# Optimization experiments

Measured on AMD Instinct MI355X. Metric: run time of the kernel, lower is better.

The kernel has to match this reference:

```python
import jax, jax.numpy as jnp
import numpy as np

B, TQ, TKV, D_MODEL, H, DQ, DV = 4, 2048, 2048, 1024, 16, 64, 64
DK = DQ

def setup_inputs() -> dict:
    key = jax.random.key(0)
    ks = jax.random.split(key, 8)
    s = 0.02
    return {
        "query_sequence": jax.random.normal(ks[0], (B, TQ, D_MODEL), jnp.float32),
        "key_value_sequence": jax.random.normal(ks[1], (B, TKV, D_MODEL), jnp.float32),
        "key_value_padding_mask": jnp.zeros((B, TKV), dtype=bool),
        "Wq": jax.random.normal(ks[2], (D_MODEL, H * DQ), jnp.float32) * s,
        "bq": jnp.zeros((H * DQ,), jnp.float32),
        "Wkv": jax.random.normal(ks[3], (D_MODEL, H * (DK + DV)), jnp.float32) * s,
        "bkv": jnp.zeros((H * (DK + DV),), jnp.float32),
        "Wo": jax.random.normal(ks[4], (H * DV, D_MODEL), jnp.float32) * s,
        "bo": jnp.zeros((D_MODEL,), jnp.float32),
        "apply_causal_mask": 1,
    }

def reference(query_sequence, key_value_sequence, key_value_padding_mask,
              Wq, bq, Wkv, bkv, Wo, bo, apply_causal_mask):
    b, tq, _ = query_sequence.shape
    tkv = key_value_sequence.shape[1]
    q = (query_sequence @ Wq + bq).reshape(b, tq, H, DQ)          # (B,Tq,H,Dq)
    kv = key_value_sequence @ Wkv + bkv
    k = kv[..., : H * DK].reshape(b, tkv, H, DK)                   # (B,Tkv,H,Dk)
    v = kv[..., H * DK :].reshape(b, tkv, H, DV)                   # (B,Tkv,H,Dv)
    scores = jnp.einsum("bqhd,bkhd->bhqk", q, k) / jnp.sqrt(jnp.float32(DK))
    neg_inf = jnp.float32(-jnp.inf)
    scores = jnp.where(key_value_padding_mask[:, None, None, :], neg_inf, scores)
    if apply_causal_mask:
        causal = jnp.tril(jnp.ones((tq, tkv), dtype=bool))
        scores = jnp.where(causal[None, None, :, :], scores, neg_inf)
    attn = jax.nn.softmax(scores, axis=-1)
    out = jnp.einsum("bhqk,bkhd->bqhd", attn, v).reshape(b, tq, H * DV)
    return out @ Wo + bo
```

## Files before the change

kernel.cpp:

```cpp
#include <hip/hip_runtime.h>
#include <hip/hip_bf16.h>

#define B_   4
#define TQ_  2048
#define TKV_ 2048
#define DM_  1024
#define H_   16
#define DH_  64

#define SC_FOLD 0.18033688011112042f

using f32x4  = __attribute__((ext_vector_type(4))) float;
using f32x16 = __attribute__((ext_vector_type(16))) float;
using s16x8  = __attribute__((ext_vector_type(8))) short;

static __device__ __forceinline__ unsigned short f2bf(float f) {
  union { float f; unsigned int u; } v; v.f = f;
  unsigned int r = v.u + 0x7FFFu + ((v.u >> 16) & 1u);
  return (unsigned short)(r >> 16);
}
static __device__ __forceinline__ unsigned int pk2(float a, float b) {
  unsigned int r;
  asm("v_cvt_pk_bf16_f32 %0, %1, %2" : "=v"(r) : "v"(a), "v"(b));
  return r;
}
static __device__ __forceinline__ float max3f(float a, float b, float c) {
  float r;
  asm("v_max3_f32 %0, %1, %2, %3" : "=v"(r) : "v"(a), "v"(b), "v"(c));
  return r;
}

#define GL16(g, l)                                                          \
  __builtin_amdgcn_global_load_lds(                                         \
      (const __attribute__((address_space(1))) unsigned int*)(g),           \
      (__attribute__((address_space(3))) unsigned int*)(l), 16, 0, 0)

__global__ __launch_bounds__(256) void k_transpose_cast(
    const float* __restrict__ W, unsigned short* __restrict__ WT, int K, int N,
    float scale) {
  __shared__ float t[64][65];
  int n0 = blockIdx.x * 64, k0 = blockIdx.y * 64;
  int tx = threadIdx.x & 63, ty = threadIdx.x >> 6;
#pragma unroll
  for (int i = 0; i < 64; i += 4)
    t[ty + i][tx] = W[(size_t)(k0 + ty + i) * N + n0 + tx];
  __syncthreads();
#pragma unroll
  for (int i = 0; i < 64; i += 4)
    WT[(size_t)(n0 + ty + i) * K + k0 + tx] = f2bf(t[tx][ty + i] * scale);
}

__global__ __launch_bounds__(256) void k_cast_bf16(
    const float* __restrict__ in, unsigned short* __restrict__ out, int n4) {
  for (int i = blockIdx.x * 256 + threadIdx.x; i < n4; i += gridDim.x * 256) {
    f32x4 v = *(const f32x4*)(in + (size_t)i * 4);
    unsigned long long u = (unsigned long long)pk2(v[0], v[1]) |
                           ((unsigned long long)pk2(v[2], v[3]) << 32);
    *(unsigned long long*)(out + (size_t)i * 4) = u;
  }
}

template <int MODE, int BN>
__global__ __launch_bounds__(512, 2) void k_gemm8(
    const unsigned short* __restrict__ A, const unsigned short* __restrict__ BT,
    const float* __restrict__ bias, float bscale, unsigned short* __restrict__ out_a,
    unsigned short* __restrict__ out_b, float* __restrict__ out_f, int Kd) {
  constexpr int NI = BN / 64;
  constexpr int NH = NI / 2;
  __shared__ __align__(16) unsigned short As[2 * 256 * 64];
  __shared__ __align__(16) unsigned short Bs[2 * BN * 64];
  const int tid = threadIdx.x, lane = tid & 63, w = tid >> 6;
  const int wm = w >> 2, wn = w & 3;

  int nwg = gridDim.x * gridDim.y;
  int bid = blockIdx.y * gridDim.x + blockIdx.x;
  int cpx = nwg >> 3;
  int sw = (bid & 7) * cpx + (bid >> 3);
  int bx = sw % gridDim.x, by = sw / gridDim.x;
  int m0 = by * 256, n0 = bx * BN;

  const int strow = tid >> 3;
  const int sx = ((tid & 7) << 4) ^ ((strow & 7) << 4);
  const char* gA = (const char*)(A + (size_t)(m0 + strow) * Kd) + sx;
  const char* gB = (const char*)(BT + (size_t)(n0 + strow) * Kd) + sx;
  char* lA = (char*)As;
  char* lB = (char*)Bs;

#define ST_A(bf, c, k0) \
  GL16(gA + ((size_t)(c) * 64 * Kd + (size_t)(k0)) * 2, lA + (bf) * 32768 + (c) * 8192 + tid * 16)
#define ST_B(bf, c, k0) \
  GL16(gB + ((size_t)(c) * 64 * Kd + (size_t)(k0)) * 2, lB + (bf) * (BN * 128) + (c) * 8192 + tid * 16)

  f32x4 acc[8][NI];
#pragma unroll
  for (int i = 0; i < 8; ++i)
#pragma unroll
    for (int j = 0; j < NI; ++j) acc[i][j] = (f32x4){0.f, 0.f, 0.f, 0.f};

  s16x8 afr[4][2], bfr[NI][2];
  const int arow = wm * 128 + (lane & 15);
  const int brow = wn * (NI * 16) + (lane & 15);
  const int fcol = (lane >> 4) * 16;

#define RD_A(bf, r) (*(const s16x8*)(lA + (bf) * 32768 + (r) * 128 + ((fcol + _kk * 64) ^ (((r) & 7) << 4))))
#define RD_B(bf, r) (*(const s16x8*)(lB + (bf) * (BN * 128) + (r) * 128 + ((fcol + _kk * 64) ^ (((r) & 7) << 4))))

  const int nT = Kd >> 6;

  ST_B(0, 0, 0); ST_B(0, 1, 0);
  if (BN == 256) { ST_B(0, 2, 0); ST_B(0, 3, 0); }
  ST_A(0, 0, 0); ST_A(0, 2, 0);
  ST_A(0, 1, 0); ST_A(0, 3, 0);
  asm volatile("s_waitcnt vmcnt(2)" ::: "memory");
  __builtin_amdgcn_s_barrier();

#pragma unroll 1
  for (int t = 0; t < nT; ++t) {
    const int cur = t & 1, nxt = cur ^ 1;
    const int k1 = (t + 1) << 6;
    const bool st = (t + 1 < nT);

#pragma unroll
    for (int mi = 0; mi < 4; ++mi)
#pragma unroll
      for (int _kk = 0; _kk < 2; ++_kk) afr[mi][_kk] = RD_A(cur, arow + mi * 16);
#pragma unroll
    for (int ni = 0; ni < NH; ++ni)
#pragma unroll
      for (int _kk = 0; _kk < 2; ++_kk) bfr[ni][_kk] = RD_B(cur, brow + ni * 16);
    if (st) { ST_B(nxt, 0, k1); ST_B(nxt, 1, k1); }
    __builtin_amdgcn_s_barrier();
    __builtin_amdgcn_s_setprio(1);
#pragma unroll
    for (int mi = 0; mi < 4; ++mi)
#pragma unroll
      for (int ni = 0; ni < NH; ++ni)
#pragma unroll
        for (int kk = 0; kk < 2; ++kk)
          acc[mi][ni] = __builtin_amdgcn_mfma_f32_16x16x32_bf16(afr[mi][kk], bfr[ni][kk], acc[mi][ni], 0, 0, 0);
    __builtin_amdgcn_s_setprio(0);
    __builtin_amdgcn_s_barrier();

#pragma unroll
    for (int ni = NH; ni < NI; ++ni)
#pragma unroll
      for (int _kk = 0; _kk < 2; ++_kk) bfr[ni][_kk] = RD_B(cur, brow + ni * 16);
    if (st) {
      if (BN == 256) { ST_B(nxt, 2, k1); ST_B(nxt, 3, k1); }
      else           { ST_A(nxt, 0, k1); ST_A(nxt, 2, k1); }
    }
    if (st) asm volatile("s_waitcnt vmcnt(4)" ::: "memory");
    else    asm volatile("s_waitcnt vmcnt(0)" ::: "memory");
    __builtin_amdgcn_s_barrier();
    __builtin_amdgcn_s_setprio(1);
#pragma unroll
    for (int mi = 0; mi < 4; ++mi)
#pragma unroll
      for (int ni = NH; ni < NI; ++ni)
#pragma unroll
        for (int kk = 0; kk < 2; ++kk)
          acc[mi][ni] = __builtin_amdgcn_mfma_f32_16x16x32_bf16(afr[mi][kk], bfr[ni][kk], acc[mi][ni], 0, 0, 0);
    __builtin_amdgcn_s_setprio(0);
    __builtin_amdgcn_s_barrier();

#pragma unroll
    for (int mi = 0; mi < 4; ++mi)
#pragma unroll
      for (int _kk = 0; _kk < 2; ++_kk) afr[mi][_kk] = RD_A(cur, arow + (mi + 4) * 16);
    if (st) {
      if (BN == 256) { ST_A(nxt, 0, k1); ST_A(nxt, 2, k1); }
      else           { ST_A(nxt, 1, k1); ST_A(nxt, 3, k1); }
    }
    __builtin_amdgcn_s_barrier();
    __builtin_amdgcn_s_setprio(1);
#pragma unroll
    for (int mi = 0; mi < 4; ++mi)
#pragma unroll
      for (int ni = 0; ni < NH; ++ni)
#pragma unroll
        for (int kk = 0; kk < 2; ++kk)
          acc[mi + 4][ni] = __builtin_amdgcn_mfma_f32_16x16x32_bf16(afr[mi][kk], bfr[ni][kk], acc[mi + 4][ni], 0, 0, 0);
    __builtin_amdgcn_s_setprio(0);
    __builtin_amdgcn_s_barrier();

    if (st && BN == 256) { ST_A(nxt, 1, k1); ST_A(nxt, 3, k1); }
    asm volatile("s_waitcnt vmcnt(2)" ::: "memory");
    __builtin_amdgcn_s_barrier();
    __builtin_amdgcn_s_setprio(1);
#pragma unroll
    for (int mi = 0; mi < 4; ++mi)
#pragma unroll
      for (int ni = NH; ni < NI; ++ni)
#pragma unroll
        for (int kk = 0; kk < 2; ++kk)
          acc[mi + 4][ni] = __builtin_amdgcn_mfma_f32_16x16x32_bf16(afr[mi][kk], bfr[ni][kk], acc[mi + 4][ni], 0, 0, 0);
    __builtin_amdgcn_s_setprio(0);
    __builtin_amdgcn_s_barrier();
  }

#pragma unroll
  for (int mi = 0; mi < 8; ++mi) {
#pragma unroll
    for (int ni = 0; ni < NI; ++ni) {
      int col = n0 + wn * (NI * 16) + ni * 16 + (lane & 15);
      int rbase = m0 + wm * 128 + mi * 16 + (lane >> 4) * 4;
      float bv = bias[col] * bscale;
      if (MODE == 1 && col >= H_ * DH_) {
        int c2 = col - H_ * DH_;
        int h = c2 >> 6, d = c2 & 63;
        int b = rbase >> 11, tt = rbase & 2047;
        union { unsigned short h4[4]; unsigned long long u; } p;
#pragma unroll
        for (int r = 0; r < 4; ++r) p.h4[r] = f2bf(acc[mi][ni][r] + bv);
        *(unsigned long long*)(out_b + ((((size_t)b * H_ + h) * DH_ + d) * TKV_ + tt)) = p.u;
      } else {
#pragma unroll
        for (int r = 0; r < 4; ++r) {
          float v = acc[mi][ni][r] + bv;
          int m = rbase + r;
          if (MODE == 0) {
            int b = m >> 11, tt = m & 2047;
            int h = col >> 6, d = col & 63;
            out_a[(((size_t)b * H_ + h) * TQ_ + tt) * DH_ + d] = f2bf(v);
          } else if (MODE == 1) {
            int b = m >> 11, tt = m & 2047;
            int h = col >> 6, d = col & 63;
            out_a[(((size_t)b * H_ + h) * TKV_ + tt) * DH_ + d] = f2bf(v);
          } else {
            out_f[(size_t)m * DM_ + col] = v;
          }
        }
      }
    }
  }
#undef ST_A
#undef ST_B
#undef RD_A
#undef RD_B
}

__global__ __launch_bounds__(256, 2) void k_attn(
    const unsigned short* __restrict__ Qb, const unsigned short* __restrict__ Kb,
    const unsigned short* __restrict__ Vtb, const unsigned char* __restrict__ mask,
    const int* __restrict__ cflag, unsigned short* __restrict__ Ob) {
  __shared__ __align__(16) unsigned short Kt[128 * 64];
  __shared__ __align__(16) unsigned short Vt[64 * 128];
  __shared__ float bias_lds[128];
  __shared__ float red[4][32];
  __shared__ int s_any;

  int bid = blockIdx.y * gridDim.x + blockIdx.x;
  int r8 = bid & 7, q8 = bid >> 3;
  int bh = r8 * 8 + (q8 >> 3);
  int bx = q8 & 7;

  int b = bh >> 4, h = bh & 15;
  int tid = threadIdx.x, lane = tid & 63, w = tid >> 6;
  int hi = lane >> 5, l31 = lane & 31, l7 = lane & 7;
  const unsigned short* Qp = Qb + (size_t)bh * TQ_ * DH_;
  const char* Kp = (const char*)(Kb + (size_t)bh * TKV_ * DH_);
  const char* Vp = (const char*)(Vtb + (size_t)bh * DH_ * TKV_);
  const unsigned char* mp = mask + (size_t)b * TKV_;
  int causal = cflag[0];
  char* kbase = (char*)Kt;
  char* vbase = (char*)Vt;

  int st_r4 = tid >> 2;
  int st_c4 = (tid & 3) * 16;
  s16x8 pKr[4], pVr[4];

#define LOAD_KV(kv0)                                                          \
  {                                                                           \
    _Pragma("unroll")                                                         \
    for (int p = 0; p < 4; ++p) {                                             \
      int krow = (p >> 1) * 64 + st_r4;                                       \
      int kx = st_c4 + (p & 1) * 64;                                          \
      pKr[p] = *(const s16x8*)(Kp + ((size_t)((kv0) + krow) * 128 + kx));     \
      int vx = st_c4 + p * 64;                                                \
      pVr[p] = *(const s16x8*)(Vp + (((size_t)st_r4 * TKV_ + (kv0)) * 2 + vx)); \
    }                                                                         \
  }
#define WRITE_KV()                                                            \
  {                                                                           \
    _Pragma("unroll")                                                         \
    for (int p = 0; p < 4; ++p) {                                             \
      int krow = (p >> 1) * 64 + st_r4;                                       \
      int kx = st_c4 + (p & 1) * 64;                                          \
      *(s16x8*)(kbase + krow * 128 + (kx ^ ((st_r4 & 7) << 4))) = pKr[p];     \
      int vx = st_c4 + p * 64;                                                \
      *(s16x8*)(vbase + st_r4 * 256 + (vx ^ ((st_r4 & 7) << 4))) = pVr[p];    \
    }                                                                         \
  }

  if (tid == 0) s_any = 0;
  __syncthreads();
  {
    int any = 0;
    for (int i = tid; i < TKV_; i += 256) any |= mp[i];
    if (any) s_any = 1;
  }
  __syncthreads();
  const int has_mask = s_any;

#pragma unroll 1
  for (int pass = 0; pass < 2; ++pass) {
    int qb = (pass ? (15 - bx) : bx) * 128;
    int qw = qb + w * 32;
    int qrow = qw + l31;

    s16x8 bQ[4];
#pragma unroll
    for (int kk = 0; kk < 4; ++kk)
      bQ[kk] = *(const s16x8*)(Qp + (size_t)qrow * DH_ + kk * 16 + hi * 8);

    f32x16 accO[2];
#pragma unroll
    for (int i = 0; i < 16; ++i) { accO[0][i] = 0.f; accO[1][i] = 0.f; }
    float m_run = -INFINITY, l_run = 0.f;

    int nT = (causal ? (qb + 128) : TKV_) >> 7;

    LOAD_KV(0);
    WRITE_KV();
    if (has_mask && tid < 128) bias_lds[tid] = mp[tid] ? -1e30f : 0.0f;
    __syncthreads();

#pragma unroll 1
    for (int it = 0; it < nT; ++it) {
      int kv0 = it << 7;
      if (it + 1 < nT) LOAD_KV(kv0 + 128);

      int nact = 4;
      if (causal) {
        int rem = qw + 31 - kv0;
        nact = rem < 0 ? 0 : ((rem >> 5) + 1);
        if (nact > 4) nact = 4;
      }

      if (nact > 0) {
        f32x16 sT[4];
        __builtin_amdgcn_s_setprio(1);
#pragma unroll
        for (int s = 0; s < 4; ++s) {
          if (s < nact) {
#pragma unroll
            for (int i = 0; i < 16; ++i) sT[s][i] = 0.f;
#pragma unroll
            for (int kk = 0; kk < 4; ++kk) {
              s16x8 aK = *(const s16x8*)(kbase + (s * 32 + l31) * 128 +
                                         ((kk * 32 + hi * 16) ^ (l7 << 4)));
              sT[s] = __builtin_amdgcn_mfma_f32_32x32x16_bf16(aK, bQ[kk], sT[s], 0, 0, 0);
            }
          }
        }
        __builtin_amdgcn_s_setprio(0);

        float a0 = -INFINITY, a1 = -INFINITY, a2 = -INFINITY, a3 = -INFINITY;
#pragma unroll
        for (int s = 0; s < 4; ++s) {
          if (s < nact) {
            int diag_s = causal && (kv0 + s * 32 + 31 > qw);
            if (diag_s || has_mask) {
#pragma unroll
              for (int r = 0; r < 16; ++r) {
                int kvloc = s * 32 + (r & 3) + 8 * (r >> 2) + 4 * hi;
                float sv = sT[s][r];
                if (has_mask) sv += bias_lds[kvloc];
                if (diag_s && (kv0 + kvloc) > qrow) sv = -1e30f;
                sT[s][r] = sv;
              }
            }
#pragma unroll
            for (int r = 0; r < 16; r += 4) {
              a0 = fmaxf(a0, sT[s][r + 0]); a1 = fmaxf(a1, sT[s][r + 1]);
              a2 = fmaxf(a2, sT[s][r + 2]); a3 = fmaxf(a3, sT[s][r + 3]);
            }
          }
        }
        float mx = max3f(max3f(a0, a1, a2), a3, -3.0e30f);
        mx = fmaxf(mx, __shfl_xor(mx, 32));

        if (!__all(mx - m_run <= 8.0f)) {
          float mnew = fmaxf(m_run, mx);
          float sc_o = exp2f(m_run - mnew);
          m_run = mnew;
          l_run *= sc_o;
          red[w][l31] = sc_o;
#pragma unroll
          for (int r = 0; r < 16; ++r) {
            float f = red[w][(r & 3) + 8 * (r >> 2) + 4 * hi];
            accO[0][r] *= f;
            accO[1][r] *= f;
          }
        }

        float s0acc = 0.f, s1acc = 0.f, s2acc = 0.f, s3acc = 0.f;
#pragma unroll
        for (int s = 0; s < 4; ++s) {
          if (s < nact) {
#pragma unroll
            for (int r = 0; r < 16; r += 4) {
              float p0 = exp2f(sT[s][r + 0] - m_run);
              float p1 = exp2f(sT[s][r + 1] - m_run);
              float p2 = exp2f(sT[s][r + 2] - m_run);
              float p3 = exp2f(sT[s][r + 3] - m_run);
              sT[s][r + 0] = p0; sT[s][r + 1] = p1;
              sT[s][r + 2] = p2; sT[s][r + 3] = p3;
              s0acc += p0; s1acc += p1; s2acc += p2; s3acc += p3;
            }
          }
        }
        float ls = (s0acc + s1acc) + (s2acc + s3acc);
        ls += __shfl_xor(ls, 32);
        l_run += ls;

#pragma unroll
        for (int c = 0; c < 8; ++c) {
          if ((c >> 1) < nact) {
            int s = c >> 1, kk = c & 1;
            unsigned int x0 = pk2(sT[s][8 * kk + 0], sT[s][8 * kk + 1]);
            unsigned int y0 = pk2(sT[s][8 * kk + 2], sT[s][8 * kk + 3]);
            unsigned int x1 = pk2(sT[s][8 * kk + 4], sT[s][8 * kk + 5]);
            unsigned int y1 = pk2(sT[s][8 * kk + 6], sT[s][8 * kk + 7]);
            unsigned int sx0 = __shfl_xor(x0, 32), sy0 = __shfl_xor(y0, 32);
            unsigned int sx1 = __shfl_xor(x1, 32), sy1 = __shfl_xor(y1, 32);
            union { unsigned int u[4]; s16x8 v; } pf;
            pf.u[0] = hi ? sx1 : x0;
            pf.u[1] = hi ? sy1 : y0;
            pf.u[2] = hi ? x1 : sx0;
            pf.u[3] = hi ? y1 : sy0;
            __builtin_amdgcn_s_setprio(1);
#pragma unroll
            for (int dt = 0; dt < 2; ++dt) {
              s16x8 vf = *(const s16x8*)(vbase + (dt * 32 + l31) * 256 +
                                         ((c * 32 + hi * 16) ^ (l7 << 4)));
              accO[dt] = __builtin_amdgcn_mfma_f32_32x32x16_bf16(pf.v, vf, accO[dt], 0, 0, 0);
            }
            __builtin_amdgcn_s_setprio(0);
          }
        }
      }

      __syncthreads();
      if (it + 1 < nT) {
        WRITE_KV();
        if (has_mask && tid < 128) bias_lds[tid] = mp[kv0 + 128 + tid] ? -1e30f : 0.0f;
      }
      __syncthreads();
    }

    red[w][l31] = 1.0f / l_run;
#pragma unroll
    for (int r = 0; r < 16; ++r) {
      int R = (r & 3) + 8 * (r >> 2) + 4 * hi;
      float f = red[w][R];
      int qg = qw + R;
      size_t base = ((size_t)b * TQ_ + qg) * DM_ + h * DH_ + l31;
      Ob[base] = f2bf(accO[0][r] * f);
      Ob[base + 32] = f2bf(accO[1][r] * f);
    }
  }
#undef LOAD_KV
#undef WRITE_KV
}

extern "C" void kernel_launch(void* const* d_in, const int* in_sizes, int n_in,
                              void* d_out, int out_size, void* d_ws, size_t ws_size,
                              hipStream_t stream) {
  const float* xq  = (const float*)d_in[0];
  const float* xkv = (const float*)d_in[1];
  const unsigned char* mask = (const unsigned char*)d_in[2];
  const float* Wq  = (const float*)d_in[3];
  const float* bq  = (const float*)d_in[4];
  const float* Wkv = (const float*)d_in[5];
  const float* bkv = (const float*)d_in[6];
  const float* Wo  = (const float*)d_in[7];
  const float* bo  = (const float*)d_in[8];
  const int* cflag = (const int*)d_in[9];
  float* out = (float*)d_out;

  char* ws = (char*)d_ws;
  unsigned short* WqT  = (unsigned short*)(ws);
  unsigned short* WkvT = (unsigned short*)(ws + ((size_t)2 << 20));
  unsigned short* WoT  = (unsigned short*)(ws + ((size_t)6 << 20));
  unsigned short* Qb   = (unsigned short*)(ws + ((size_t)8 << 20));
  unsigned short* Kb   = (unsigned short*)(ws + ((size_t)24 << 20));
  unsigned short* Vb   = (unsigned short*)(ws + ((size_t)40 << 20));
  unsigned short* Xr   = (unsigned short*)(ws + ((size_t)56 << 20));
  unsigned short* Ob   = Xr;

  k_transpose_cast<<<dim3(16, 16), 256, 0, stream>>>(Wq, WqT, 1024, 1024, SC_FOLD);
  k_transpose_cast<<<dim3(32, 16), 256, 0, stream>>>(Wkv, WkvT, 1024, 2048, 1.0f);
  k_transpose_cast<<<dim3(16, 16), 256, 0, stream>>>(Wo, WoT, 1024, 1024, 1.0f);

  k_cast_bf16<<<2048, 256, 0, stream>>>(xq, Xr, B_ * TQ_ * DM_ / 4);
  k_gemm8<0, 128><<<dim3(8, 32), 512, 0, stream>>>(Xr, WqT, bq, SC_FOLD, Qb, nullptr, nullptr, 1024);

  k_cast_bf16<<<2048, 256, 0, stream>>>(xkv, Xr, B_ * TKV_ * DM_ / 4);
  k_gemm8<1, 256><<<dim3(8, 32), 512, 0, stream>>>(Xr, WkvT, bkv, 1.0f, Kb, Vb, nullptr, 1024);

  k_attn<<<dim3(8, B_ * H_), 256, 0, stream>>>(Qb, Kb, Vb, mask, cflag, Ob);

  k_gemm8<2, 128><<<dim3(8, 32), 512, 0, stream>>>(Ob, WoT, bo, 1.0f, nullptr, nullptr, out, 1024);
}
```

Baseline: 200.5 us.

## Read K/V fragments directly from global memory instead of staging through LDS

Removes the shared-memory staging of K and V tiles (register prefetch, swizzled LDS writes, and two block barriers per iteration) in the attention kernel. Each wave now loads its MFMA operand fragments straight from global memory and skips inactive causal tiles with a per-wave continue. This drops barrier and LDS traffic and frees LDS for occupancy, but each of the four waves re-fetches the same K/V data from global/L2, with no software prefetch to hide latency.

New measurement: 264.1 us. +31.7%, slower.

```diff
diff --git a/kernel.cpp b/kernel.cpp
--- a/kernel.cpp
+++ b/kernel.cpp
@@ -243,9 +243,6 @@
     const unsigned short* __restrict__ Qb, const unsigned short* __restrict__ Kb,
     const unsigned short* __restrict__ Vtb, const unsigned char* __restrict__ mask,
     const int* __restrict__ cflag, unsigned short* __restrict__ Ob) {
-  __shared__ __align__(16) unsigned short Kt[128 * 64];
-  __shared__ __align__(16) unsigned short Vt[64 * 128];
-  __shared__ float bias_lds[128];
   __shared__ float red[4][32];
   __shared__ int s_any;
 
@@ -256,41 +253,12 @@
 
   int b = bh >> 4, h = bh & 15;
   int tid = threadIdx.x, lane = tid & 63, w = tid >> 6;
-  int hi = lane >> 5, l31 = lane & 31, l7 = lane & 7;
+  int hi = lane >> 5, l31 = lane & 31;
   const unsigned short* Qp = Qb + (size_t)bh * TQ_ * DH_;
-  const char* Kp = (const char*)(Kb + (size_t)bh * TKV_ * DH_);
-  const char* Vp = (const char*)(Vtb + (size_t)bh * DH_ * TKV_);
+  const unsigned short* Kp = Kb + (size_t)bh * TKV_ * DH_;
+  const unsigned short* Vp = Vtb + (size_t)bh * DH_ * TKV_;
   const unsigned char* mp = mask + (size_t)b * TKV_;
   int causal = cflag[0];
-  char* kbase = (char*)Kt;
-  char* vbase = (char*)Vt;
-
-  int st_r4 = tid >> 2;
-  int st_c4 = (tid & 3) * 16;
-  s16x8 pKr[4], pVr[4];
-
-#define LOAD_KV(kv0)                                                          \
-  {                                                                           \
-    _Pragma("unroll")                                                         \
-    for (int p = 0; p < 4; ++p) {                                             \
-      int krow = (p >> 1) * 64 + st_r4;                                       \
-      int kx = st_c4 + (p & 1) * 64;                                          \
-      pKr[p] = *(const s16x8*)(Kp + ((size_t)((kv0) + krow) * 128 + kx));     \
-      int vx = st_c4 + p * 64;                                                \
-      pVr[p] = *(const s16x8*)(Vp + (((size_t)st_r4 * TKV_ + (kv0)) * 2 + vx)); \
-    }                                                                         \
-  }
-#define WRITE_KV()                                                            \
-  {                                                                           \
-    _Pragma("unroll")                                                         \
-    for (int p = 0; p < 4; ++p) {                                             \
-      int krow = (p >> 1) * 64 + st_r4;                                       \
-      int kx = st_c4 + (p & 1) * 64;                                          \
-      *(s16x8*)(kbase + krow * 128 + (kx ^ ((st_r4 & 7) << 4))) = pKr[p];     \
-      int vx = st_c4 + p * 64;                                                \
-      *(s16x8*)(vbase + st_r4 * 256 + (vx ^ ((st_r4 & 7) << 4))) = pVr[p];    \
-    }                                                                         \
-  }
 
   if (tid == 0) s_any = 0;
   __syncthreads();
@@ -320,15 +288,9 @@
 
     int nT = (causal ? (qb + 128) : TKV_) >> 7;
 
-    LOAD_KV(0);
-    WRITE_KV();
-    if (has_mask && tid < 128) bias_lds[tid] = mp[tid] ? -1e30f : 0.0f;
-    __syncthreads();
-
 #pragma unroll 1
     for (int it = 0; it < nT; ++it) {
       int kv0 = it << 7;
-      if (it + 1 < nT) LOAD_KV(kv0 + 128);
 
       int nact = 4;
       if (causal) {
@@ -336,117 +298,109 @@
         nact = rem < 0 ? 0 : ((rem >> 5) + 1);
         if (nact > 4) nact = 4;
       }
-
-      if (nact > 0) {
-        f32x16 sT[4];
-        __builtin_amdgcn_s_setprio(1);
-#pragma unroll
-        for (int s = 0; s < 4; ++s) {
-          if (s < nact) {
-#pragma unroll
-            for (int i = 0; i < 16; ++i) sT[s][i] = 0.f;
-#pragma unroll
-            for (int kk = 0; kk < 4; ++kk) {
-              s16x8 aK = *(const s16x8*)(kbase + (s * 32 + l31) * 128 +
-                                         ((kk * 32 + hi * 16) ^ (l7 << 4)));
-              sT[s] = __builtin_amdgcn_mfma_f32_32x32x16_bf16(aK, bQ[kk], sT[s], 0, 0, 0);
+      if (nact == 0) continue;
+
+      f32x16 sT[4];
+#pragma unroll
+      for (int s = 0; s < 4; ++s) {
+        if (s < nact) {
+#pragma unroll
+          for (int i = 0; i < 16; ++i) sT[s][i] = 0.f;
+          __builtin_amdgcn_s_setprio(1);
+#pragma unroll
+          for (int kk = 0; kk < 4; ++kk) {
+            s16x8 aK = *(const s16x8*)(Kp + (size_t)(kv0 + s * 32 + l31) * DH_ +
+                                       kk * 16 + hi * 8);
+            sT[s] = __builtin_amdgcn_mfma_f32_32x32x16_bf16(aK, bQ[kk], sT[s], 0, 0, 0);
+          }
+          __builtin_amdgcn_s_setprio(0);
+        }
+      }
+
+      float a0 = -INFINITY, a1 = -INFINITY, a2 = -INFINITY, a3 = -INFINITY;
+#pragma unroll
+      for (int s = 0; s < 4; ++s) {
+        if (s < nact) {
+          int diag_s = causal && (kv0 + s * 32 + 31 > qw);
+          if (diag_s || has_mask) {
+#pragma unroll
+            for (int r = 0; r < 16; ++r) {
+              int kvloc = s * 32 + (r & 3) + 8 * (r >> 2) + 4 * hi;
+              float sv = sT[s][r];
+              if (has_mask) sv += (mp[kv0 + kvloc] ? -1e30f : 0.0f);
+              if (diag_s && (kv0 + kvloc) > qrow) sv = -1e30f;
+              sT[s][r] = sv;
             }
           }
-        }
-        __builtin_amdgcn_s_setprio(0);
-
-        float a0 = -INFINITY, a1 = -INFINITY, a2 = -INFINITY, a3 = -INFINITY;
-#pragma unroll
-        for (int s = 0; s < 4; ++s) {
-          if (s < nact) {
-            int diag_s = causal && (kv0 + s * 32 + 31 > qw);
-            if (diag_s || has_mask) {
-#pragma unroll
-              for (int r = 0; r < 16; ++r) {
-                int kvloc = s * 32 + (r & 3) + 8 * (r >> 2) + 4 * hi;
-                float sv = sT[s][r];
-                if (has_mask) sv += bias_lds[kvloc];
-                if (diag_s && (kv0 + kvloc) > qrow) sv = -1e30f;
-                sT[s][r] = sv;
-              }
-            }
-#pragma unroll
-            for (int r = 0; r < 16; r += 4) {
-              a0 = fmaxf(a0, sT[s][r + 0]); a1 = fmaxf(a1, sT[s][r + 1]);
-              a2 = fmaxf(a2, sT[s][r + 2]); a3 = fmaxf(a3, sT[s][r + 3]);
-            }
-          }
-        }
-        float mx = max3f(max3f(a0, a1, a2), a3, -3.0e30f);
-        mx = fmaxf(mx, __shfl_xor(mx, 32));
-
-        if (!__all(mx - m_run <= 8.0f)) {
-          float mnew = fmaxf(m_run, mx);
-          float sc_o = exp2f(m_run - mnew);
-          m_run = mnew;
-          l_run *= sc_o;
-          red[w][l31] = sc_o;
-#pragma unroll
-          for (int r = 0; r < 16; ++r) {
-            float f = red[w][(r & 3) + 8 * (r >> 2) + 4 * hi];
-            accO[0][r] *= f;
-            accO[1][r] *= f;
-          }
-        }
-
-        float s0acc = 0.f, s1acc = 0.f, s2acc = 0.f, s3acc = 0.f;
-#pragma unroll
-        for (int s = 0; s < 4; ++s) {
-          if (s < nact) {
-#pragma unroll
-            for (int r = 0; r < 16; r += 4) {
-              float p0 = exp2f(sT[s][r + 0] - m_run);
-              float p1 = exp2f(sT[s][r + 1] - m_run);
-              float p2 = exp2f(sT[s][r + 2] - m_run);
-              float p3 = exp2f(sT[s][r + 3] - m_run);
-              sT[s][r + 0] = p0; sT[s][r + 1] = p1;
-              sT[s][r + 2] = p2; sT[s][r + 3] = p3;
-              s0acc += p0; s1acc += p1; s2acc += p2; s3acc += p3;
-            }
-          }
-        }
-        float ls = (s0acc + s1acc) + (s2acc + s3acc);
-        ls += __shfl_xor(ls, 32);
-        l_run += ls;
-
-#pragma unroll
-        for (int c = 0; c < 8; ++c) {
-          if ((c >> 1) < nact) {
-            int s = c >> 1, kk = c & 1;
-            unsigned int x0 = pk2(sT[s][8 * kk + 0], sT[s][8 * kk + 1]);
-            unsigned int y0 = pk2(sT[s][8 * kk + 2], sT[s][8 * kk + 3]);
-            unsigned int x1 = pk2(sT[s][8 * kk + 4], sT[s][8 * kk + 5]);
-            unsigned int y1 = pk2(sT[s][8 * kk + 6], sT[s][8 * kk + 7]);
-            unsigned int sx0 = __shfl_xor(x0, 32), sy0 = __shfl_xor(y0, 32);
-            unsigned int sx1 = __shfl_xor(x1, 32), sy1 = __shfl_xor(y1, 32);
-            union { unsigned int u[4]; s16x8 v; } pf;
-            pf.u[0] = hi ? sx1 : x0;
-            pf.u[1] = hi ? sy1 : y0;
-            pf.u[2] = hi ? x1 : sx0;
-            pf.u[3] = hi ? y1 : sy0;
-            __builtin_amdgcn_s_setprio(1);
-#pragma unroll
-            for (int dt = 0; dt < 2; ++dt) {
-              s16x8 vf = *(const s16x8*)(vbase + (dt * 32 + l31) * 256 +
-                                         ((c * 32 + hi * 16) ^ (l7 << 4)));
-              accO[dt] = __builtin_amdgcn_mfma_f32_32x32x16_bf16(pf.v, vf, accO[dt], 0, 0, 0);
-            }
-            __builtin_amdgcn_s_setprio(0);
-          }
-        }
-      }
-
-      __syncthreads();
-      if (it + 1 < nT) {
-        WRITE_KV();
-        if (has_mask && tid < 128) bias_lds[tid] = mp[kv0 + 128 + tid] ? -1e30f : 0.0f;
-      }
-      __syncthreads();
+#pragma unroll
+          for (int r = 0; r < 16; r += 4) {
+            a0 = fmaxf(a0, sT[s][r + 0]); a1 = fmaxf(a1, sT[s][r + 1]);
+            a2 = fmaxf(a2, sT[s][r + 2]); a3 = fmaxf(a3, sT[s][r + 3]);
+          }
+        }
+      }
+      float mx = max3f(max3f(a0, a1, a2), a3, -3.0e30f);
+      mx = fmaxf(mx, __shfl_xor(mx, 32));
+
+      if (!__all(mx - m_run <= 8.0f)) {
+        float mnew = fmaxf(m_run, mx);
+        float sc_o = exp2f(m_run - mnew);
+        m_run = mnew;
+        l_run *= sc_o;
+        red[w][l31] = sc_o;
+#pragma unroll
+        for (int r = 0; r < 16; ++r) {
+          float f = red[w][(r & 3) + 8 * (r >> 2) + 4 * hi];
+          accO[0][r] *= f;
+          accO[1][r] *= f;
+        }
+      }
+
+      float s0acc = 0.f, s1acc = 0.f, s2acc = 0.f, s3acc = 0.f;
+#pragma unroll
+      for (int s = 0; s < 4; ++s) {
+        if (s < nact) {
+#pragma unroll
+          for (int r = 0; r < 16; r += 4) {
+            float p0 = exp2f(sT[s][r + 0] - m_run);
+            float p1 = exp2f(sT[s][r + 1] - m_run);
+            float p2 = exp2f(sT[s][r + 2] - m_run);
+            float p3 = exp2f(sT[s][r + 3] - m_run);
+            sT[s][r + 0] = p0; sT[s][r + 1] = p1;
+            sT[s][r + 2] = p2; sT[s][r + 3] = p3;
+            s0acc += p0; s1acc += p1; s2acc += p2; s3acc += p3;
+          }
+        }
+      }
+      float ls = (s0acc + s1acc) + (s2acc + s3acc);
+      ls += __shfl_xor(ls, 32);
+      l_run += ls;
+
+#pragma unroll
+      for (int c = 0; c < 8; ++c) {
+        if ((c >> 1) < nact) {
+          int s = c >> 1, kk = c & 1;
+          unsigned int x0 = pk2(sT[s][8 * kk + 0], sT[s][8 * kk + 1]);
+          unsigned int y0 = pk2(sT[s][8 * kk + 2], sT[s][8 * kk + 3]);
+          unsigned int x1 = pk2(sT[s][8 * kk + 4], sT[s][8 * kk + 5]);
+          unsigned int y1 = pk2(sT[s][8 * kk + 6], sT[s][8 * kk + 7]);
+          unsigned int sx0 = __shfl_xor(x0, 32), sy0 = __shfl_xor(y0, 32);
+          unsigned int sx1 = __shfl_xor(x1, 32), sy1 = __shfl_xor(y1, 32);
+          union { unsigned int u[4]; s16x8 v; } pf;
+          pf.u[0] = hi ? sx1 : x0;
+          pf.u[1] = hi ? sy1 : y0;
+          pf.u[2] = hi ? x1 : sx0;
+          pf.u[3] = hi ? y1 : sy0;
+          __builtin_amdgcn_s_setprio(1);
+#pragma unroll
+          for (int dt = 0; dt < 2; ++dt) {
+            s16x8 vf = *(const s16x8*)(Vp + (size_t)(dt * 32 + l31) * TKV_ +
+                                       kv0 + c * 16 + hi * 8);
+            accO[dt] = __builtin_amdgcn_mfma_f32_32x32x16_bf16(pf.v, vf, accO[dt], 0, 0, 0);
+          }
+          __builtin_amdgcn_s_setprio(0);
+        }
+      }
     }
 
     red[w][l31] = 1.0f / l_run;
@@ -460,8 +414,6 @@
       Ob[base + 32] = f2bf(accO[1][r] * f);
     }
   }
-#undef LOAD_KV
-#undef WRITE_KV
 }
 
 extern "C" void kernel_launch(void* const* d_in, const int* in_sizes, int n_in,
```
